# Kernel tuning notes

Hardware: AMD Instinct MI355X
Metric: run time of the kernel (lower is better)

## Reference

```python
import jax, jax.numpy as jnp
import numpy as np

RANK = 8
ALPHA = 16.0
SCALING = ALPHA / RANK  # 2.0
B, S, DIN, DOUT = 4, 4096, 4096, 4096


def setup_inputs() -> dict:
    key = jax.random.key(0)
    k = jax.random.split(key, 6)
    return {
        "x": jax.random.normal(k[0], (B, S, DIN), dtype=jnp.float32),
        "codes": jax.random.normal(k[1], (B, S, RANK), dtype=jnp.float32),
        "W": jax.random.normal(k[2], (DOUT, DIN), dtype=jnp.float32) * 0.02,
        "b": jax.random.normal(k[3], (DOUT,), dtype=jnp.float32) * 0.02,
        "lora_U": jax.random.normal(k[4], (DOUT, RANK), dtype=jnp.float32) * 0.02,
        "lora_V": jax.random.normal(k[5], (DIN, RANK), dtype=jnp.float32) * 0.02,
    }


def reference(x, codes, W, b, lora_U, lora_V):
    # base linear: x @ W^T + b  -> [B, S, DOUT]
    base = jnp.einsum("bsi,oi->bso", x, W) + b
    # generated low-rank update: (x @ V) gated by per-token codes, then @ U^T
    xv = jnp.einsum("bsi,ir->bsr", x, lora_V)          # [B, S, rank]
    lora = jnp.einsum("bsr,or->bso", xv * codes, lora_U)  # [B, S, DOUT]
    return base + lora * SCALING
```

## Files before the change

kernel.cpp:

```cpp
#include <hip/hip_runtime.h>
#include <hip/hip_bf16.h>


typedef __bf16 bf16_t;
typedef __bf16 bf16x8 __attribute__((ext_vector_type(8)));
typedef float f32x4 __attribute__((ext_vector_type(4)));

#define M_TOT 16384
#define N_TOT 4096
#define K_TOT 4096
#define NT 64

#define GLOAD_LDS16(gp, lp)                                                    \
  __builtin_amdgcn_global_load_lds(                                            \
      (const __attribute__((address_space(1))) void*)(gp),                     \
      (__attribute__((address_space(3))) void*)(lp), 16, 0, 0)

__global__ void __launch_bounds__(256) conv_w_kernel(const float* __restrict__ W,
                                                     bf16_t* __restrict__ wbf) {
  size_t i = ((size_t)blockIdx.x * 256 + threadIdx.x) * 8;
  const float4* p = (const float4*)(W + i);
  float4 a = p[0], b = p[1];
  bf16x8 v;
  v[0] = (bf16_t)a.x; v[1] = (bf16_t)a.y; v[2] = (bf16_t)a.z; v[3] = (bf16_t)a.w;
  v[4] = (bf16_t)b.x; v[5] = (bf16_t)b.y; v[6] = (bf16_t)b.z; v[7] = (bf16_t)b.w;
  *(bf16x8*)(wbf + i) = v;
}

__global__ void __launch_bounds__(256) prep_x_kernel(
    const float* __restrict__ x, const float* __restrict__ codes,
    const float* __restrict__ V, bf16_t* __restrict__ xbf,
    float* __restrict__ g) {
  const int tid = threadIdx.x;
  const int lane = tid & 63;
  const int wv = tid >> 6;
  const int m0 = blockIdx.x * 4;
  const int c0 = tid * 16;

  float xv[4][8];
#pragma unroll
  for (int rr = 0; rr < 4; ++rr)
#pragma unroll
    for (int r = 0; r < 8; ++r) xv[rr][r] = 0.f;

#pragma unroll
  for (int h = 0; h < 2; ++h) {
    const int cb = c0 + h * 8;
    float xr[4][8];
#pragma unroll
    for (int rr = 0; rr < 4; ++rr) {
      const float4* xp = (const float4*)(x + (size_t)(m0 + rr) * K_TOT + cb);
      float4 a0 = xp[0], a1 = xp[1];
      xr[rr][0] = a0.x; xr[rr][1] = a0.y; xr[rr][2] = a0.z; xr[rr][3] = a0.w;
      xr[rr][4] = a1.x; xr[rr][5] = a1.y; xr[rr][6] = a1.z; xr[rr][7] = a1.w;
      bf16x8 bv;
#pragma unroll
      for (int t = 0; t < 8; ++t) bv[t] = (bf16_t)xr[rr][t];
      *(bf16x8*)(xbf + (size_t)(m0 + rr) * K_TOT + cb) = bv;
    }
#pragma unroll
    for (int t = 0; t < 8; ++t) {
      const float4* vp = (const float4*)(V + (size_t)(cb + t) * 8);
      float4 v0 = vp[0], v1 = vp[1];
#pragma unroll
      for (int rr = 0; rr < 4; ++rr) {
        float xi = xr[rr][t];
        xv[rr][0] += xi * v0.x; xv[rr][1] += xi * v0.y;
        xv[rr][2] += xi * v0.z; xv[rr][3] += xi * v0.w;
        xv[rr][4] += xi * v1.x; xv[rr][5] += xi * v1.y;
        xv[rr][6] += xi * v1.z; xv[rr][7] += xi * v1.w;
      }
    }
  }

  __shared__ float red[4][4][8];
#pragma unroll
  for (int rr = 0; rr < 4; ++rr)
#pragma unroll
    for (int r = 0; r < 8; ++r) {
      float v = xv[rr][r];
      for (int s = 32; s > 0; s >>= 1) v += __shfl_down(v, s);
      if (lane == 0) red[wv][rr][r] = v;
    }
  __syncthreads();
  if (tid < 32) {
    int rr = tid >> 3, r = tid & 7;
    float tot = red[0][rr][r] + red[1][rr][r] + red[2][rr][r] + red[3][rr][r];
    int m = m0 + rr;
    g[m * 8 + r] = tot * codes[(size_t)m * 8 + r] * 2.0f;
  }
}

#define BAR __builtin_amdgcn_s_barrier()
#define VMC4 asm volatile("s_waitcnt vmcnt(4)" ::: "memory")
#define VMC0 asm volatile("s_waitcnt vmcnt(0)" ::: "memory")

#define STAGE(DB, AB, HALF, KT, SRC)                                           \
  {                                                                            \
    _Pragma("unroll") for (int r_ = 0; r_ < 2; ++r_) {                         \
      int rowl_ = (HALF) * 128 + (r_ * 8 + w) * 8 + srow;                      \
      const bf16_t* gp_ = (SRC) + (size_t)rowl_ * K_TOT + (KT) * 64 + sgk;     \
      GLOAD_LDS16(gp_, &lds[(DB) * 2 + (AB)][rowl_ * 64 + sj * 8]);            \
    }                                                                          \
  }

#define READ_A(BUF, MI0, DST)                                                  \
  _Pragma("unroll") for (int mi_ = 0; mi_ < 4; ++mi_) {                        \
    DST[mi_][0] = *(const bf16x8*)&lds[(BUF) * 2][arow0 + ((MI0) + mi_) * 1024 + aslot0]; \
    DST[mi_][1] = *(const bf16x8*)&lds[(BUF) * 2][arow0 + ((MI0) + mi_) * 1024 + aslot1]; \
  }

#define READ_B(BUF, NJ0, DST)                                                  \
  _Pragma("unroll") for (int nj_ = 0; nj_ < 2; ++nj_) {                        \
    DST[nj_][0] = *(const bf16x8*)&lds[(BUF) * 2 + 1][brow0 + ((NJ0) + nj_) * 1024 + aslot0]; \
    DST[nj_][1] = *(const bf16x8*)&lds[(BUF) * 2 + 1][brow0 + ((NJ0) + nj_) * 1024 + aslot1]; \
  }

#define MFMA_Q(MI0, NJ0, ASRC, BSRC)                                           \
  __builtin_amdgcn_s_setprio(1);                                               \
  _Pragma("unroll") for (int mi_ = 0; mi_ < 4; ++mi_)                          \
  _Pragma("unroll") for (int nj_ = 0; nj_ < 2; ++nj_) {                        \
    acc[(MI0) + mi_][(NJ0) + nj_] = __builtin_amdgcn_mfma_f32_16x16x32_bf16(   \
        ASRC[mi_][0], BSRC[nj_][0], acc[(MI0) + mi_][(NJ0) + nj_], 0, 0, 0);   \
    acc[(MI0) + mi_][(NJ0) + nj_] = __builtin_amdgcn_mfma_f32_16x16x32_bf16(   \
        ASRC[mi_][1], BSRC[nj_][1], acc[(MI0) + mi_][(NJ0) + nj_], 0, 0, 0);   \
  }                                                                            \
  __builtin_amdgcn_s_setprio(0);

#define KTILE(BUF, KT, S1, S2, VM)                                             \
  if (S1) STAGE(BUF ^ 1, 0, 1, (KT) + 1, aSrc);                                \
  if ((VM) == 4) { VMC4; } else { VMC0; }                                      \
  BAR;                                                                         \
  READ_A(BUF, 0, aF);                                                          \
  READ_B(BUF, 0, b01);                                                         \
  MFMA_Q(0, 0, aF, b01);                                                       \
  READ_B(BUF, 2, b23);                                                         \
  BAR;                                                                         \
  if (S1) STAGE(BUF ^ 1, 1, 0, (KT) + 1, bSrc);                                \
  MFMA_Q(0, 2, aF, b23);                                                       \
  READ_A(BUF, 4, aG);                                                          \
  BAR;                                                                         \
  if (S1) STAGE(BUF ^ 1, 1, 1, (KT) + 1, bSrc);                                \
  MFMA_Q(4, 2, aG, b23);                                                       \
  BAR;                                                                         \
  if (S2) STAGE(BUF, 0, 0, (KT) + 2, aSrc);                                    \
  MFMA_Q(4, 0, aG, b01);                                                       \
  BAR;

__global__ void __launch_bounds__(512) gemm_kernel(
    const bf16_t* __restrict__ A,
    const bf16_t* __restrict__ Bm,
    const float* __restrict__ bias, const float* __restrict__ U,
    const float* __restrict__ g, float* __restrict__ out) {
  const int tid = threadIdx.x;
  const int lane = tid & 63;
  const int w = tid >> 6;
  const int wr = w >> 2;
  const int wc = w & 3;
  const int llo = lane & 15, lhi = lane >> 4;

  int bid = blockIdx.x;
  int sw = (bid & 7) * 128 + (bid >> 3);
  const int bm = sw >> 4;
  const int bn = sw & 15;

  __shared__ __attribute__((aligned(128))) bf16_t lds[4][16384];

  const bf16_t* aSrc = A + (size_t)bm * 256 * K_TOT;
  const bf16_t* bSrc = Bm + (size_t)bn * 256 * K_TOT;

  const int srow = lane >> 3;
  const int sj = lane & 7;
  const int sgk = (sj ^ srow) * 8;

  const int xs = llo & 7;
  const int arow0 = (wr * 128 + llo) * 64;
  const int brow0 = (wc * 64 + llo) * 64;
  const int aslot0 = ((0 + lhi) ^ xs) * 8;
  const int aslot1 = ((4 + lhi) ^ xs) * 8;

  f32x4 acc[8][4] = {};
  bf16x8 aF[4][2], aG[4][2], b01[2][2], b23[2][2];

  STAGE(0, 0, 0, 0, aSrc);
  STAGE(0, 0, 1, 0, aSrc);
  STAGE(0, 1, 0, 0, bSrc);
  STAGE(0, 1, 1, 0, bSrc);
  STAGE(1, 0, 0, 1, aSrc);

#pragma unroll 1
  for (int t = 0; t < NT - 2; t += 2) {
    KTILE(0, t, 1, 1, 4);
    KTILE(1, t + 1, 1, 1, 4);
  }
  KTILE(0, NT - 2, 1, 0, 4);
  KTILE(1, NT - 1, 0, 0, 0);

  const int n0 = bn * 256 + wc * 64;
  int nidx[4];
  float biasv[4];
  float Un[4][8];
#pragma unroll
  for (int nj = 0; nj < 4; ++nj) {
    int n = n0 + nj * 16 + llo;
    nidx[nj] = n;
    biasv[nj] = bias[n];
    const float4* up = (const float4*)(U + (size_t)n * 8);
    float4 u0 = up[0], u1 = up[1];
    Un[nj][0] = u0.x; Un[nj][1] = u0.y; Un[nj][2] = u0.z; Un[nj][3] = u0.w;
    Un[nj][4] = u1.x; Un[nj][5] = u1.y; Un[nj][6] = u1.z; Un[nj][7] = u1.w;
  }
#pragma unroll
  for (int mi = 0; mi < 8; ++mi) {
#pragma unroll
    for (int reg = 0; reg < 4; ++reg) {
      int m = bm * 256 + wr * 128 + mi * 16 + lhi * 4 + reg;
      const float4* gp = (const float4*)(g + m * 8);
      float4 g0 = gp[0], g1 = gp[1];
      float* orow = out + (size_t)m * N_TOT;
#pragma unroll
      for (int nj = 0; nj < 4; ++nj) {
        float lora = g0.x * Un[nj][0] + g0.y * Un[nj][1] + g0.z * Un[nj][2] +
                     g0.w * Un[nj][3] + g1.x * Un[nj][4] + g1.y * Un[nj][5] +
                     g1.z * Un[nj][6] + g1.w * Un[nj][7];
        orow[nidx[nj]] = acc[mi][nj][reg] + biasv[nj] + lora;
      }
    }
  }
}

__global__ void __launch_bounds__(256) naive_kernel(
    const float* __restrict__ x, const float* __restrict__ codes,
    const float* __restrict__ W, const float* __restrict__ bias,
    const float* __restrict__ U, const float* __restrict__ V,
    float* __restrict__ out) {
  int m = blockIdx.x >> 4;
  int n = ((blockIdx.x & 15) << 8) + threadIdx.x;
  const float* xr = x + (size_t)m * K_TOT;
  const float* wrow = W + (size_t)n * K_TOT;
  float acc = 0.f;
  float xv[8] = {0, 0, 0, 0, 0, 0, 0, 0};
  for (int k = 0; k < K_TOT; k += 4) {
    float4 xa = *(const float4*)(xr + k);
    float4 wa = *(const float4*)(wrow + k);
    acc += xa.x * wa.x + xa.y * wa.y + xa.z * wa.z + xa.w * wa.w;
    const float* xs = (const float*)&xa;
#pragma unroll
    for (int t = 0; t < 4; ++t) {
      const float* vrow = V + (size_t)(k + t) * 8;
      float xi = xs[t];
#pragma unroll
      for (int r = 0; r < 8; ++r) xv[r] += xi * vrow[r];
    }
  }
  float lora = 0.f;
#pragma unroll
  for (int r = 0; r < 8; ++r)
    lora += xv[r] * codes[(size_t)m * 8 + r] * U[(size_t)n * 8 + r];
  out[(size_t)m * N_TOT + n] = acc + bias[n] + 2.0f * lora;
}

extern "C" void kernel_launch(void* const* d_in, const int* in_sizes, int n_in,
                              void* d_out, int out_size, void* d_ws,
                              size_t ws_size, hipStream_t stream) {
  const float* x = (const float*)d_in[0];
  const float* codes = (const float*)d_in[1];
  const float* W = (const float*)d_in[2];
  const float* b = (const float*)d_in[3];
  const float* U = (const float*)d_in[4];
  const float* V = (const float*)d_in[5];
  float* out = (float*)d_out;

  const size_t xbf_bytes = (size_t)M_TOT * K_TOT * 2;
  const size_t wbf_bytes = (size_t)N_TOT * K_TOT * 2;
  const size_t g_bytes = (size_t)M_TOT * 8 * 4;

  if (ws_size >= xbf_bytes + wbf_bytes + g_bytes) {
    bf16_t* xbf = (bf16_t*)d_ws;
    bf16_t* wbf = (bf16_t*)((char*)d_ws + xbf_bytes);
    float* g = (float*)((char*)d_ws + xbf_bytes + wbf_bytes);
    hipLaunchKernelGGL(conv_w_kernel, dim3(8192), dim3(256), 0, stream, W, wbf);
    hipLaunchKernelGGL(prep_x_kernel, dim3(4096), dim3(256), 0, stream, x,
                       codes, V, xbf, g);
    hipLaunchKernelGGL(gemm_kernel, dim3(1024), dim3(512), 0, stream, xbf, wbf,
                       b, U, g, out);
  } else {
    hipLaunchKernelGGL(naive_kernel, dim3((M_TOT) * (N_TOT / 256)), dim3(256),
                       0, stream, x, codes, W, b, U, V, out);
  }
}
```

Baseline: 617.5 us.

## Switch GEMM inner loop from 16x16x32 to 32x32x16 bf16 MFMA tiles

```diff
diff --git a/kernel.cpp b/kernel.cpp
--- a/kernel.cpp
+++ b/kernel.cpp
@@ -4,7 +4,7 @@
 
 typedef __bf16 bf16_t;
 typedef __bf16 bf16x8 __attribute__((ext_vector_type(8)));
-typedef float f32x4 __attribute__((ext_vector_type(4)));
+typedef float f32x16 __attribute__((ext_vector_type(16)));
 
 #define M_TOT 16384
 #define N_TOT 4096
@@ -104,26 +104,27 @@
     }                                                                          \
   }
 
-#define READ_A(BUF, MI0, DST)                                                  \
-  _Pragma("unroll") for (int mi_ = 0; mi_ < 4; ++mi_) {                        \
-    DST[mi_][0] = *(const bf16x8*)&lds[(BUF) * 2][arow0 + ((MI0) + mi_) * 1024 + aslot0]; \
-    DST[mi_][1] = *(const bf16x8*)&lds[(BUF) * 2][arow0 + ((MI0) + mi_) * 1024 + aslot1]; \
-  }
-
-#define READ_B(BUF, NJ0, DST)                                                  \
-  _Pragma("unroll") for (int nj_ = 0; nj_ < 2; ++nj_) {                        \
-    DST[nj_][0] = *(const bf16x8*)&lds[(BUF) * 2 + 1][brow0 + ((NJ0) + nj_) * 1024 + aslot0]; \
-    DST[nj_][1] = *(const bf16x8*)&lds[(BUF) * 2 + 1][brow0 + ((NJ0) + nj_) * 1024 + aslot1]; \
-  }
-
-#define MFMA_Q(MI0, NJ0, ASRC, BSRC)                                           \
+#define SLOTQ(Q) ((((Q) * 2 + lq) ^ xs) * 8)
+
+#define READ_A2(BUF, MI0, DST)                                                 \
+  _Pragma("unroll") for (int mi_ = 0; mi_ < 2; ++mi_)                          \
+  _Pragma("unroll") for (int q_ = 0; q_ < 4; ++q_) {                           \
+    DST[mi_][q_] = *(const bf16x8*)&lds[(BUF) * 2]                             \
+        [arow0 + ((MI0) + mi_) * 2048 + ((((q_) * 2 + lq) ^ xs) * 8)];         \
+  }
+
+#define READ_B2(BUF, NJ, DST)                                                  \
+  _Pragma("unroll") for (int q_ = 0; q_ < 4; ++q_) {                           \
+    DST[q_] = *(const bf16x8*)&lds[(BUF) * 2 + 1]                              \
+        [brow0 + (NJ) * 2048 + ((((q_) * 2 + lq) ^ xs) * 8)];                  \
+  }
+
+#define MFMA_Q32(MI0, NJ, ASRC, BSRC)                                          \
   __builtin_amdgcn_s_setprio(1);                                               \
-  _Pragma("unroll") for (int mi_ = 0; mi_ < 4; ++mi_)                          \
-  _Pragma("unroll") for (int nj_ = 0; nj_ < 2; ++nj_) {                        \
-    acc[(MI0) + mi_][(NJ0) + nj_] = __builtin_amdgcn_mfma_f32_16x16x32_bf16(   \
-        ASRC[mi_][0], BSRC[nj_][0], acc[(MI0) + mi_][(NJ0) + nj_], 0, 0, 0);   \
-    acc[(MI0) + mi_][(NJ0) + nj_] = __builtin_amdgcn_mfma_f32_16x16x32_bf16(   \
-        ASRC[mi_][1], BSRC[nj_][1], acc[(MI0) + mi_][(NJ0) + nj_], 0, 0, 0);   \
+  _Pragma("unroll") for (int q_ = 0; q_ < 4; ++q_)                             \
+  _Pragma("unroll") for (int mi_ = 0; mi_ < 2; ++mi_) {                        \
+    acc[(MI0) + mi_][NJ] = __builtin_amdgcn_mfma_f32_32x32x16_bf16(            \
+        ASRC[mi_][q_], BSRC[q_], acc[(MI0) + mi_][NJ], 0, 0, 0);               \
   }                                                                            \
   __builtin_amdgcn_s_setprio(0);
 
@@ -131,20 +132,20 @@
   if (S1) STAGE(BUF ^ 1, 0, 1, (KT) + 1, aSrc);                                \
   if ((VM) == 4) { VMC4; } else { VMC0; }                                      \
   BAR;                                                                         \
-  READ_A(BUF, 0, aF);                                                          \
-  READ_B(BUF, 0, b01);                                                         \
-  MFMA_Q(0, 0, aF, b01);                                                       \
-  READ_B(BUF, 2, b23);                                                         \
+  READ_A2(BUF, 0, aF);                                                         \
+  READ_B2(BUF, 0, b0);                                                         \
+  MFMA_Q32(0, 0, aF, b0);                                                      \
+  READ_B2(BUF, 1, b1);                                                         \
   BAR;                                                                         \
   if (S1) STAGE(BUF ^ 1, 1, 0, (KT) + 1, bSrc);                                \
-  MFMA_Q(0, 2, aF, b23);                                                       \
-  READ_A(BUF, 4, aG);                                                          \
+  MFMA_Q32(0, 1, aF, b1);                                                      \
+  READ_A2(BUF, 2, aG);                                                         \
   BAR;                                                                         \
   if (S1) STAGE(BUF ^ 1, 1, 1, (KT) + 1, bSrc);                                \
-  MFMA_Q(4, 2, aG, b23);                                                       \
+  MFMA_Q32(2, 1, aG, b1);                                                      \
   BAR;                                                                         \
   if (S2) STAGE(BUF, 0, 0, (KT) + 2, aSrc);                                    \
-  MFMA_Q(4, 0, aG, b01);                                                       \
+  MFMA_Q32(2, 0, aG, b0);                                                      \
   BAR;
 
 __global__ void __launch_bounds__(512) gemm_kernel(
@@ -157,7 +158,9 @@
   const int w = tid >> 6;
   const int wr = w >> 2;
   const int wc = w & 3;
-  const int llo = lane & 15, lhi = lane >> 4;
+  const int l32 = lane & 31;
+  const int lq = lane >> 5;
+  const int xs = lane & 7;
 
   int bid = blockIdx.x;
   int sw = (bid & 7) * 128 + (bid >> 3);
@@ -173,14 +176,11 @@
   const int sj = lane & 7;
   const int sgk = (sj ^ srow) * 8;
 
-  const int xs = llo & 7;
-  const int arow0 = (wr * 128 + llo) * 64;
-  const int brow0 = (wc * 64 + llo) * 64;
-  const int aslot0 = ((0 + lhi) ^ xs) * 8;
-  const int aslot1 = ((4 + lhi) ^ xs) * 8;
-
-  f32x4 acc[8][4] = {};
-  bf16x8 aF[4][2], aG[4][2], b01[2][2], b23[2][2];
+  const int arow0 = (wr * 128 + l32) * 64;
+  const int brow0 = (wc * 64 + l32) * 64;
+
+  f32x16 acc[4][2] = {};
+  bf16x8 aF[2][4], aG[2][4], b0[4], b1[4];
 
   STAGE(0, 0, 0, 0, aSrc);
   STAGE(0, 0, 1, 0, aSrc);
@@ -196,14 +196,12 @@
   KTILE(0, NT - 2, 1, 0, 4);
   KTILE(1, NT - 1, 0, 0, 0);
 
-  const int n0 = bn * 256 + wc * 64;
-  int nidx[4];
-  float biasv[4];
-  float Un[4][8];
-#pragma unroll
-  for (int nj = 0; nj < 4; ++nj) {
-    int n = n0 + nj * 16 + llo;
-    nidx[nj] = n;
+  const int C0 = bn * 256 + wc * 64 + l32;
+  float biasv[2];
+  float Un[2][8];
+#pragma unroll
+  for (int nj = 0; nj < 2; ++nj) {
+    int n = C0 + nj * 32;
     biasv[nj] = bias[n];
     const float4* up = (const float4*)(U + (size_t)n * 8);
     float4 u0 = up[0], u1 = up[1];
@@ -211,19 +209,30 @@
     Un[nj][4] = u1.x; Un[nj][5] = u1.y; Un[nj][6] = u1.z; Un[nj][7] = u1.w;
   }
 #pragma unroll
-  for (int mi = 0; mi < 8; ++mi) {
-#pragma unroll
-    for (int reg = 0; reg < 4; ++reg) {
-      int m = bm * 256 + wr * 128 + mi * 16 + lhi * 4 + reg;
-      const float4* gp = (const float4*)(g + m * 8);
-      float4 g0 = gp[0], g1 = gp[1];
-      float* orow = out + (size_t)m * N_TOT;
-#pragma unroll
-      for (int nj = 0; nj < 4; ++nj) {
-        float lora = g0.x * Un[nj][0] + g0.y * Un[nj][1] + g0.z * Un[nj][2] +
-                     g0.w * Un[nj][3] + g1.x * Un[nj][4] + g1.y * Un[nj][5] +
-                     g1.z * Un[nj][6] + g1.w * Un[nj][7];
-        orow[nidx[nj]] = acc[mi][nj][reg] + biasv[nj] + lora;
+  for (int mi = 0; mi < 4; ++mi) {
+#pragma unroll
+    for (int h = 0; h < 4; ++h) {
+      const int r0 = bm * 256 + wr * 128 + mi * 32 + 4 * lq + 8 * h;
+      float gv[4][8];
+#pragma unroll
+      for (int rr = 0; rr < 4; ++rr) {
+        const float4* gp = (const float4*)(g + (size_t)(r0 + rr) * 8);
+        float4 g0 = gp[0], g1 = gp[1];
+        gv[rr][0] = g0.x; gv[rr][1] = g0.y; gv[rr][2] = g0.z; gv[rr][3] = g0.w;
+        gv[rr][4] = g1.x; gv[rr][5] = g1.y; gv[rr][6] = g1.z; gv[rr][7] = g1.w;
+      }
+#pragma unroll
+      for (int nj = 0; nj < 2; ++nj) {
+#pragma unroll
+        for (int rr = 0; rr < 4; ++rr) {
+          const int reg = h * 4 + rr;
+          float lora = gv[rr][0] * Un[nj][0] + gv[rr][1] * Un[nj][1] +
+                       gv[rr][2] * Un[nj][2] + gv[rr][3] * Un[nj][3] +
+                       gv[rr][4] * Un[nj][4] + gv[rr][5] * Un[nj][5] +
+                       gv[rr][6] * Un[nj][6] + gv[rr][7] * Un[nj][7];
+          out[(size_t)(r0 + rr) * N_TOT + C0 + nj * 32] =
+              acc[mi][nj][reg] + biasv[nj] + lora;
+        }
       }
     }
   }
```

Result: slower. 726.5 us (+17.7%).
